# Optimization experiments

Hardware: AMD Instinct MI355X
Metric: run time of the kernel (lower is better)

Reference implementation:

```python
import jax, jax.numpy as jnp
import numpy as np

TILE = 16
CLIP_NEAR, CLIP_FAR = 0.01, 10.0


def _sqrt_keepnan(x):
    # forward: sqrt(x) for x>0, NaN otherwise (matches torch.sqrt on negatives);
    # double-where keeps gradients finite.
    pos = x > 0
    return jnp.where(pos, jnp.sqrt(jnp.where(pos, x, 1.0)), jnp.nan)


def _quat_to_rot(q):
    # faithful to the source _quat_to_rot (including its sign quirks)
    x, y, z, w = q[:, 0], q[:, 1], q[:, 2], q[:, 3]
    r0 = jnp.stack([1 - 2 * (y * y + z * z), 2 * (x * y - w * z), 2 * (x * z + w * y)], -1)
    r1 = jnp.stack([2 * (x * y + w * z), 1 - 2 * (x * x - z * z), 2 * (y * z - w * x)], -1)
    r2 = jnp.stack([2 * (x * z + w * y), 2 * (y * z + w * x), 1 - 2 * (x * x + y * y)], -1)
    return jnp.stack([r0, r1, r2], -2)  # (N,3,3)


def _forward(mu, scales, quats, cols, opcs, viewmat, focal, H, W):
    N = mu.shape[0]
    fx = fy = float(focal)
    cx, cy = W / 2.0, H / 2.0
    n_, f_ = CLIP_NEAR, CLIP_FAR

    # --- project gaussians ---
    t = viewmat @ jnp.concatenate([mu.T, jnp.ones((1, N), mu.dtype)], 0)  # (4,N) camera space
    tp0 = (2.0 * fx / W) * t[0]
    tp1 = (2.0 * fy / H) * t[1]
    tp2 = ((f_ + n_) / (f_ - n_)) * t[2] + (-2.0 * f_ * n_ / (f_ - n_)) * t[3]
    tp3 = t[2]
    xys = jnp.stack([W * tp0 / tp3 / 2 + cx, H * tp1 / tp3 / 2 + cy], 1)  # (N,2)
    depths = tp2

    R = _quat_to_rot(quats)
    RS = R * scales[:, None, :]              # R @ diag(s)
    Sigma = RS @ jnp.swapaxes(RS, 1, 2)      # (N,3,3)
    tz = t[2]
    zz = jnp.zeros_like(tz)
    J = jnp.stack([
        jnp.stack([fx / tz, zz, -fx * t[0] / tz ** 2], -1),
        jnp.stack([zz, fy / tz, -fy * t[1] / tz ** 2], -1)], -2)  # (N,2,3)
    Rcw = viewmat[:3, :3]
    M = jnp.einsum('nij,jk->nik', J, Rcw)
    covs = jnp.einsum('nij,njk,nlk->nil', M, Sigma, M)  # (N,2,2)

    ind = jnp.argsort(depths)                # depth sort (front-to-back)
    xys, covs = xys[ind], covs[ind]
    cols_s, opcs_s = cols[ind], opcs[ind]

    # --- bounding boxes -> tile membership mask ---
    a, b, d = covs[:, 0, 0], covs[:, 0, 1], covs[:, 1, 1]
    Aev = jnp.sqrt(a * a - 2 * a * d + 4 * b * b + d * d)
    Bev = a + d
    l1, l2 = 0.5 * (Aev + Bev), 0.5 * (Bev - Aev)
    r1 = 3.0 * _sqrt_keepnan(l1)
    r2 = 3.0 * _sqrt_keepnan(l2)
    mx, my = xys[:, 0], xys[:, 1]
    corners = jnp.stack([
        jnp.stack([mx - r1, my + r2], -1),
        jnp.stack([mx + r1, my + r2], -1),
        jnp.stack([mx + r1, my - r2], -1),
        jnp.stack([mx - r1, my - r2], -1)], 1)  # (N,4,2)
    theta = jnp.where(b != 0, jnp.arctan2(l1 - a, b),
                      jnp.where(a >= d, jnp.pi / 2, 0.0))
    cth, sth = jnp.cos(theta), jnp.sin(theta)
    rot = jnp.stack([jnp.stack([cth, -sth], -1), jnp.stack([sth, cth], -1)], -2)
    bm = corners.mean(1, keepdims=True)
    bbs = jnp.einsum('nij,nkj->nki', rot, corners - bm) + bm
    bbs = jnp.where(jnp.isnan(bbs), -1.0, bbs)
    Wt, Ht = W // TILE, H // TILE
    xmin = jnp.clip(jnp.floor(bbs[:, :, 0].min(1) / TILE), 0, Wt - 1).astype(jnp.int32)
    xmax = jnp.clip(jnp.ceil(bbs[:, :, 0].max(1) / TILE), 0, Wt - 1).astype(jnp.int32)
    ymin = jnp.clip(jnp.floor(bbs[:, :, 1].min(1) / TILE), 0, Ht - 1).astype(jnp.int32)
    ymax = jnp.clip(jnp.ceil(bbs[:, :, 1].max(1) / TILE), 0, Ht - 1).astype(jnp.int32)
    txi = jnp.arange(Wt)
    tyi = jnp.arange(Ht)
    tmask = ((txi[None, None, :] >= xmin[:, None, None]) & (txi[None, None, :] <= xmax[:, None, None]) &
             (tyi[None, :, None] >= ymin[:, None, None]) & (tyi[None, :, None] <= ymax[:, None, None]))  # (N,Ht,Wt)
    pmask = jnp.moveaxis(jnp.repeat(jnp.repeat(tmask, TILE, 1), TILE, 2), 0, -1)  # (H,W,N)

    # --- rasterize: per-pixel gaussian eval + sorted alpha compositing ---
    e = 1e-6
    det = (a + e) * (d + e) - covs[:, 0, 1] * covs[:, 1, 0]
    i00 = (d + e) / det
    i01 = -covs[:, 0, 1] / det
    i10 = -covs[:, 1, 0] / det
    i11 = (a + e) / det
    px = jnp.arange(W, dtype=mu.dtype)
    py = jnp.arange(H, dtype=mu.dtype)
    dx = px[None, :, None] - mx[None, None, :]   # (1,W,N)
    dy = py[:, None, None] - my[None, None, :]   # (H,1,N)
    quad = dx * (i00 * dx + i01 * dy) + dy * (i10 * dx + i11 * dy)  # (H,W,N)
    Pg = jnp.nan_to_num(jnp.exp(-0.5 * quad))
    O = jax.nn.sigmoid(jax.nn.sigmoid(opcs_s))   # double sigmoid: faithful to source
    alpha = O[None, None, :] * Pg
    alpha = jnp.where(pmask, alpha, 0.0)         # only gaussians binned to this tile
    alpha = jnp.where(alpha < 0.001, 0.0, alpha)
    alpha = jnp.minimum(alpha, 0.99)
    trans = jnp.cumprod(1.0 - alpha, -1)         # inclusive transmittance
    Dtr = jnp.concatenate([jnp.ones((H, W, 1), alpha.dtype), trans[..., :-1]], -1)
    C = jnp.clip(cols_s, 1e-4, 1.0)
    rgb = jnp.clip(jnp.einsum('hwn,nc->hwc', alpha * Dtr, C), 1e-4, 1.0)
    nonempty = jnp.repeat(jnp.repeat(tmask.any(0), TILE, 0), TILE, 1)  # empty tiles stay 0
    return jnp.where(nonempty[..., None], rgb, 0.0)


def setup_inputs() -> dict:
    key = jax.random.key(0)
    ks = jax.random.split(key, 6)
    N, H, W = 512, 256, 256
    mu = jax.random.normal(ks[0], (N, 3), jnp.float32)
    scales = jax.random.uniform(ks[1], (N, 3), jnp.float32) * 0.05 + 0.01
    q = jax.random.normal(ks[2], (N, 4), jnp.float32)
    quats = q / jnp.linalg.norm(q, axis=1, keepdims=True)
    cols = jax.random.uniform(ks[3], (N, 3), jnp.float32)
    opcs = jax.random.normal(ks[4], (N,), jnp.float32)
    viewmat = jnp.array([[1, 0, 0, 0], [0, 1, 0, 0], [0, 0, 1, 5.0], [0, 0, 0, 1]], jnp.float32)
    gt = jax.random.uniform(ks[5], (H, W, 3), jnp.float32)
    return {"mu": mu, "scales": scales, "quats": quats, "cols": cols, "opcs": opcs,
            "viewmat": viewmat, "gt": gt, "focal": 200, "H": H, "W": W}


def reference(mu, scales, quats, cols, opcs, viewmat, gt, focal, H, W):
    # gt is accepted (matches source signature) but unused by forward
    return _forward(mu, scales, quats, cols, opcs, viewmat, focal, H, W)
```

## Files before the change

### kernel.cpp

```cpp
#include <hip/hip_runtime.h>
#include <math.h>
#include <float.h>

#define NMAX 512
#define TILE 16
#define FDIV(a,b) __fdividef((a),(b))

__global__ __launch_bounds__(512) void fused_kernel(
    const float* __restrict__ mu, const float* __restrict__ scales,
    const float* __restrict__ quats, const float* __restrict__ cols,
    const float* __restrict__ opcs, const float* __restrict__ vm,
    const int* __restrict__ focal_p, const int* __restrict__ H_p,
    const int* __restrict__ W_p, float* __restrict__ out, int N)
{
    __shared__ float s_mx[NMAX], s_my[NMAX];
    __shared__ float s_i00[NMAX], s_i01[NMAX], s_i10[NMAX], s_i11[NMAX];
    __shared__ float s_O[NMAX], s_c0[NMAX], s_c1[NMAX], s_c2[NMAX];
    __shared__ unsigned int s_key[NMAX];
    __shared__ int s_list[NMAX];
    __shared__ unsigned long long s_lk[NMAX];
    __shared__ int s_sorted[NMAX];
    __shared__ float s_pr[256], s_pg[256], s_pb[256], s_pT[256];
    __shared__ int s_cnt;

    const int lt = threadIdx.x;
    const int p  = lt & 255;
    const int hv = lt >> 8;
    const int tx = blockIdx.x, ty = blockIdx.y;

    if (lt == 0) s_cnt = 0;
    __syncthreads();

    const int   Wi = W_p[0], Hi = H_p[0];
    const float fx = (float)focal_p[0];
    const float fy = fx;
    const float Wf = (float)Wi, Hf = (float)Hi;
    const float cxf = (float)((double)Wi / 2.0);
    const float cyf = (float)((double)Hi / 2.0);
    const float sxc = (float)(2.0 * (double)fx / (double)Wi);
    const float syc = (float)(2.0 * (double)fy / (double)Hi);
    const float dc1 = (float)((10.0 + 0.01) / (10.0 - 0.01));
    const float dc2 = (float)(-2.0 * 10.0 * 0.01 / (10.0 - 0.01));
    const int Wt = Wi / TILE, Ht = Hi / TILE;

    const int g = lt;
    if (g < N) {
        const float m0 = mu[3*g], m1 = mu[3*g+1], m2 = mu[3*g+2];
        const float t0 = vm[0]*m0  + vm[1]*m1  + vm[2]*m2  + vm[3];
        const float t1 = vm[4]*m0  + vm[5]*m1  + vm[6]*m2  + vm[7];
        const float t2 = vm[8]*m0  + vm[9]*m1  + vm[10]*m2 + vm[11];
        const float t3 = vm[12]*m0 + vm[13]*m1 + vm[14]*m2 + vm[15];

        const float depth = dc1 * t2 + dc2 * t3;
        unsigned int ub = __float_as_uint(depth);
        ub = (ub & 0x80000000u) ? ~ub : (ub | 0x80000000u);
        s_key[g] = ub;

        const float mx = FDIV(Wf * (sxc * t0), t2) * 0.5f + cxf;
        const float my = FDIV(Hf * (syc * t1), t2) * 0.5f + cyf;

        const float4 q = ((const float4*)quats)[g];
        const float qx = q.x, qy = q.y, qz = q.z, qw = q.w;
        const float R00 = 1.0f - 2.0f*(qy*qy + qz*qz);
        const float R01 = 2.0f*(qx*qy - qw*qz);
        const float R02 = 2.0f*(qx*qz + qw*qy);
        const float R10 = 2.0f*(qx*qy + qw*qz);
        const float R11 = 1.0f - 2.0f*(qx*qx - qz*qz);
        const float R12 = 2.0f*(qy*qz - qw*qx);
        const float R20 = 2.0f*(qx*qz + qw*qy);
        const float R21 = 2.0f*(qy*qz + qw*qx);
        const float R22 = 1.0f - 2.0f*(qx*qx + qy*qy);

        const float s0 = scales[3*g], s1 = scales[3*g+1], s2 = scales[3*g+2];
        const float A00 = R00*s0, A01 = R01*s1, A02 = R02*s2;
        const float A10 = R10*s0, A11 = R11*s1, A12 = R12*s2;
        const float A20 = R20*s0, A21 = R21*s1, A22 = R22*s2;
        const float S00 = A00*A00 + A01*A01 + A02*A02;
        const float S01 = A00*A10 + A01*A11 + A02*A12;
        const float S02 = A00*A20 + A01*A21 + A02*A22;
        const float S11 = A10*A10 + A11*A11 + A12*A12;
        const float S12 = A10*A20 + A11*A21 + A12*A22;
        const float S22 = A20*A20 + A21*A21 + A22*A22;

        const float tz = t2;
        const float J00 = FDIV(fx, tz);
        const float J02 = FDIV(-fx * t0, tz * tz);
        const float J11 = FDIV(fy, tz);
        const float J12 = FDIV(-fy * t1, tz * tz);
        const float M00 = J00*vm[0] + J02*vm[8];
        const float M01 = J00*vm[1] + J02*vm[9];
        const float M02 = J00*vm[2] + J02*vm[10];
        const float M10 = J11*vm[4] + J12*vm[8];
        const float M11 = J11*vm[5] + J12*vm[9];
        const float M12 = J11*vm[6] + J12*vm[10];
        const float T00 = M00*S00 + M01*S01 + M02*S02;
        const float T01 = M00*S01 + M01*S11 + M02*S12;
        const float T02 = M00*S02 + M01*S12 + M02*S22;
        const float T10 = M10*S00 + M11*S01 + M12*S02;
        const float T11 = M10*S01 + M11*S11 + M12*S12;
        const float T12 = M10*S02 + M11*S12 + M12*S22;
        const float a   = T00*M00 + T01*M01 + T02*M02;
        const float b   = T00*M10 + T01*M11 + T02*M12;
        const float c10 = T10*M00 + T11*M01 + T12*M02;
        const float d   = T10*M10 + T11*M11 + T12*M12;

        const float Aev = sqrtf(a*a - 2.0f*a*d + 4.0f*b*b + d*d);
        const float Bev = a + d;
        const float l1 = 0.5f * (Aev + Bev);
        const float l2 = 0.5f * (Bev - Aev);
        const float r1 = (l1 > 0.0f) ? 3.0f * sqrtf(l1) : NAN;
        const float r2 = (l2 > 0.0f) ? 3.0f * sqrtf(l2) : NAN;

        float cth, sth;
        if (b != 0.0f) {
            const float yv = l1 - a;
            const float h  = sqrtf(b*b + yv*yv);
            cth = FDIV(b,  h);
            sth = FDIV(yv, h);
        } else if (a >= d) {
            cth = -4.371139e-8f;
            sth = 1.0f;
        } else {
            cth = 1.0f;
            sth = 0.0f;
        }

        const float crx[4] = { mx - r1, mx + r1, mx + r1, mx - r1 };
        const float cry[4] = { my + r2, my + r2, my - r2, my - r2 };
        const float bmx = (((crx[0] + crx[1]) + crx[2]) + crx[3]) * 0.25f;
        const float bmy = (((cry[0] + cry[1]) + cry[2]) + cry[3]) * 0.25f;

        float xmn = FLT_MAX, xmxv = -FLT_MAX, ymn = FLT_MAX, ymxv = -FLT_MAX;
        #pragma unroll
        for (int k = 0; k < 4; ++k) {
            const float ox = crx[k] - bmx, oy = cry[k] - bmy;
            float bx = (cth*ox + (-sth)*oy) + bmx;
            float by = (sth*ox + cth*oy) + bmy;
            if (isnan(bx)) bx = -1.0f;
            if (isnan(by)) by = -1.0f;
            xmn = fminf(xmn, bx); xmxv = fmaxf(xmxv, bx);
            ymn = fminf(ymn, by); ymxv = fmaxf(ymxv, by);
        }
        const int xmin = (int)fminf(fmaxf(floorf(xmn  * 0.0625f), 0.0f), (float)(Wt - 1));
        const int xmax = (int)fminf(fmaxf(ceilf (xmxv * 0.0625f), 0.0f), (float)(Wt - 1));
        const int ymin = (int)fminf(fmaxf(floorf(ymn  * 0.0625f), 0.0f), (float)(Ht - 1));
        const int ymax = (int)fminf(fmaxf(ceilf (ymxv * 0.0625f), 0.0f), (float)(Ht - 1));

        const float e = 1e-06f;
        const float det = (a + e) * (d + e) - b * c10;
        const float idet = FDIV(1.0f, det);
        s_i00[g] = (d + e) * idet;
        s_i01[g] = -b   * idet;
        s_i10[g] = -c10 * idet;
        s_i11[g] = (a + e) * idet;

        const float op  = opcs[g];
        const float sg1 = FDIV(1.0f, 1.0f + __expf(-op));
        s_O[g] = FDIV(1.0f, 1.0f + __expf(-sg1));

        s_c0[g] = fminf(fmaxf(cols[3*g    ], 1e-04f), 1.0f);
        s_c1[g] = fminf(fmaxf(cols[3*g + 1], 1e-04f), 1.0f);
        s_c2[g] = fminf(fmaxf(cols[3*g + 2], 1e-04f), 1.0f);
        s_mx[g] = mx; s_my[g] = my;

        if (tx >= xmin && tx <= xmax && ty >= ymin && ty <= ymax) {
            const int pos = atomicAdd(&s_cnt, 1);
            s_list[pos] = g;
        }
    }
    __syncthreads();
    const int M = s_cnt;

    for (int t = lt; t < M; t += 512) {
        const int gi = s_list[t];
        s_lk[t] = ((unsigned long long)s_key[gi] << 32) | (unsigned int)gi;
    }
    __syncthreads();
    for (int t = lt; t < M; t += 512) {
        const unsigned long long mine = s_lk[t];
        int rank = 0;
        for (int s = 0; s < M; ++s) rank += (s_lk[s] < mine) ? 1 : 0;
        s_sorted[rank] = (int)(mine & 0xFFFFFFFFu);
    }
    __syncthreads();

    const int W  = gridDim.x * TILE;
    const int px = tx * TILE + (p & 15);
    const int py = ty * TILE + (p >> 4);
    const float fpx = (float)px, fpy = (float)py;

    const int Mh = (M + 1) >> 1;
    const int j0 = hv ? Mh : 0;
    const int j1 = hv ? M  : Mh;

    float Tt = 1.0f, rr = 0.0f, gg = 0.0f, bb = 0.0f;
    for (int j = j0; j < j1; ++j) {
        const int n = s_sorted[j];
        const float dx = fpx - s_mx[n];
        const float dy = fpy - s_my[n];
        const float quad = dx * (s_i00[n]*dx + s_i01[n]*dy)
                         + dy * (s_i10[n]*dx + s_i11[n]*dy);
        float Pg = __expf(-0.5f * quad);
        if (isnan(Pg)) Pg = 0.0f;
        float alpha = s_O[n] * Pg;
        if (alpha < 0.001f) continue;
        alpha = fminf(alpha, 0.99f);
        const float wgt = alpha * Tt;
        rr += wgt * s_c0[n];
        gg += wgt * s_c1[n];
        bb += wgt * s_c2[n];
        Tt *= (1.0f - alpha);
    }

    if (hv == 1) { s_pr[p] = rr; s_pg[p] = gg; s_pb[p] = bb; s_pT[p] = Tt; }
    __syncthreads();

    if (hv == 0) {
        rr += Tt * s_pr[p];
        gg += Tt * s_pg[p];
        bb += Tt * s_pb[p];

        const int o = (py * W + px) * 3;
        if (M > 0) {
            out[o    ] = fminf(fmaxf(rr, 1e-04f), 1.0f);
            out[o + 1] = fminf(fmaxf(gg, 1e-04f), 1.0f);
            out[o + 2] = fminf(fmaxf(bb, 1e-04f), 1.0f);
        } else {
            out[o] = 0.0f; out[o + 1] = 0.0f; out[o + 2] = 0.0f;
        }
    }
}

extern "C" void kernel_launch(void* const* d_in, const int* in_sizes, int n_in,
                              void* d_out, int out_size, void* d_ws, size_t ws_size,
                              hipStream_t stream) {
    const float* mu     = (const float*)d_in[0];
    const float* scales = (const float*)d_in[1];
    const float* quats  = (const float*)d_in[2];
    const float* cols   = (const float*)d_in[3];
    const float* opcs   = (const float*)d_in[4];
    const float* vm     = (const float*)d_in[5];
    const int* focal_p  = (const int*)d_in[7];
    const int* H_p      = (const int*)d_in[8];
    const int* W_p      = (const int*)d_in[9];

    const int N = in_sizes[4];
    const int HW = out_size / 3;
    int W = (int)(sqrt((double)HW) + 0.5);
    int H = HW / W;

    dim3 grid(W / TILE, H / TILE), block(512);
    fused_kernel<<<grid, block, 0, stream>>>(mu, scales, quats, cols, opcs, vm,
                                             focal_p, H_p, W_p, (float*)d_out, N);
}
```

Measured before the change: 17.60 us.

## Split per-gaussian preprocessing into a separate kernel and compact lists via ballot

Per-gaussian projection, covariance, bounding-box and opacity math now runs once in a prep kernel that writes to workspace, instead of being recomputed redundantly in each of the 256 tile blocks. The render kernel reads packed tile bounds, builds its per-tile list with wave ballot/popcount instead of shared atomics, and gathers parameters into shared memory in sorted order so the blend loop indexes directly without indirection. The cost is a second kernel launch and a global-memory round trip through the workspace.

```diff
diff --git a/kernel.cpp b/kernel.cpp
--- a/kernel.cpp
+++ b/kernel.cpp
@@ -6,30 +6,16 @@
 #define TILE 16
 #define FDIV(a,b) __fdividef((a),(b))
 
-__global__ __launch_bounds__(512) void fused_kernel(
+
+__global__ __launch_bounds__(256) void prep_kernel(
     const float* __restrict__ mu, const float* __restrict__ scales,
     const float* __restrict__ quats, const float* __restrict__ cols,
     const float* __restrict__ opcs, const float* __restrict__ vm,
     const int* __restrict__ focal_p, const int* __restrict__ H_p,
-    const int* __restrict__ W_p, float* __restrict__ out, int N)
+    const int* __restrict__ W_p, float* __restrict__ ws, int N)
 {
-    __shared__ float s_mx[NMAX], s_my[NMAX];
-    __shared__ float s_i00[NMAX], s_i01[NMAX], s_i10[NMAX], s_i11[NMAX];
-    __shared__ float s_O[NMAX], s_c0[NMAX], s_c1[NMAX], s_c2[NMAX];
-    __shared__ unsigned int s_key[NMAX];
-    __shared__ int s_list[NMAX];
-    __shared__ unsigned long long s_lk[NMAX];
-    __shared__ int s_sorted[NMAX];
-    __shared__ float s_pr[256], s_pg[256], s_pb[256], s_pT[256];
-    __shared__ int s_cnt;
-
-    const int lt = threadIdx.x;
-    const int p  = lt & 255;
-    const int hv = lt >> 8;
-    const int tx = blockIdx.x, ty = blockIdx.y;
-
-    if (lt == 0) s_cnt = 0;
-    __syncthreads();
+    const int g = blockIdx.x * 256 + threadIdx.x;
+    if (g >= N) return;
 
     const int   Wi = W_p[0], Hi = H_p[0];
     const float fx = (float)focal_p[0];
@@ -43,147 +29,194 @@
     const float dc2 = (float)(-2.0 * 10.0 * 0.01 / (10.0 - 0.01));
     const int Wt = Wi / TILE, Ht = Hi / TILE;
 
-    const int g = lt;
-    if (g < N) {
-        const float m0 = mu[3*g], m1 = mu[3*g+1], m2 = mu[3*g+2];
-        const float t0 = vm[0]*m0  + vm[1]*m1  + vm[2]*m2  + vm[3];
-        const float t1 = vm[4]*m0  + vm[5]*m1  + vm[6]*m2  + vm[7];
-        const float t2 = vm[8]*m0  + vm[9]*m1  + vm[10]*m2 + vm[11];
-        const float t3 = vm[12]*m0 + vm[13]*m1 + vm[14]*m2 + vm[15];
-
-        const float depth = dc1 * t2 + dc2 * t3;
-        unsigned int ub = __float_as_uint(depth);
-        ub = (ub & 0x80000000u) ? ~ub : (ub | 0x80000000u);
-        s_key[g] = ub;
-
-        const float mx = FDIV(Wf * (sxc * t0), t2) * 0.5f + cxf;
-        const float my = FDIV(Hf * (syc * t1), t2) * 0.5f + cyf;
-
-        const float4 q = ((const float4*)quats)[g];
-        const float qx = q.x, qy = q.y, qz = q.z, qw = q.w;
-        const float R00 = 1.0f - 2.0f*(qy*qy + qz*qz);
-        const float R01 = 2.0f*(qx*qy - qw*qz);
-        const float R02 = 2.0f*(qx*qz + qw*qy);
-        const float R10 = 2.0f*(qx*qy + qw*qz);
-        const float R11 = 1.0f - 2.0f*(qx*qx - qz*qz);
-        const float R12 = 2.0f*(qy*qz - qw*qx);
-        const float R20 = 2.0f*(qx*qz + qw*qy);
-        const float R21 = 2.0f*(qy*qz + qw*qx);
-        const float R22 = 1.0f - 2.0f*(qx*qx + qy*qy);
-
-        const float s0 = scales[3*g], s1 = scales[3*g+1], s2 = scales[3*g+2];
-        const float A00 = R00*s0, A01 = R01*s1, A02 = R02*s2;
-        const float A10 = R10*s0, A11 = R11*s1, A12 = R12*s2;
-        const float A20 = R20*s0, A21 = R21*s1, A22 = R22*s2;
-        const float S00 = A00*A00 + A01*A01 + A02*A02;
-        const float S01 = A00*A10 + A01*A11 + A02*A12;
-        const float S02 = A00*A20 + A01*A21 + A02*A22;
-        const float S11 = A10*A10 + A11*A11 + A12*A12;
-        const float S12 = A10*A20 + A11*A21 + A12*A22;
-        const float S22 = A20*A20 + A21*A21 + A22*A22;
-
-        const float tz = t2;
-        const float J00 = FDIV(fx, tz);
-        const float J02 = FDIV(-fx * t0, tz * tz);
-        const float J11 = FDIV(fy, tz);
-        const float J12 = FDIV(-fy * t1, tz * tz);
-        const float M00 = J00*vm[0] + J02*vm[8];
-        const float M01 = J00*vm[1] + J02*vm[9];
-        const float M02 = J00*vm[2] + J02*vm[10];
-        const float M10 = J11*vm[4] + J12*vm[8];
-        const float M11 = J11*vm[5] + J12*vm[9];
-        const float M12 = J11*vm[6] + J12*vm[10];
-        const float T00 = M00*S00 + M01*S01 + M02*S02;
-        const float T01 = M00*S01 + M01*S11 + M02*S12;
-        const float T02 = M00*S02 + M01*S12 + M02*S22;
-        const float T10 = M10*S00 + M11*S01 + M12*S02;
-        const float T11 = M10*S01 + M11*S11 + M12*S12;
-        const float T12 = M10*S02 + M11*S12 + M12*S22;
-        const float a   = T00*M00 + T01*M01 + T02*M02;
-        const float b   = T00*M10 + T01*M11 + T02*M12;
-        const float c10 = T10*M00 + T11*M01 + T12*M02;
-        const float d   = T10*M10 + T11*M11 + T12*M12;
-
-        const float Aev = sqrtf(a*a - 2.0f*a*d + 4.0f*b*b + d*d);
-        const float Bev = a + d;
-        const float l1 = 0.5f * (Aev + Bev);
-        const float l2 = 0.5f * (Bev - Aev);
-        const float r1 = (l1 > 0.0f) ? 3.0f * sqrtf(l1) : NAN;
-        const float r2 = (l2 > 0.0f) ? 3.0f * sqrtf(l2) : NAN;
-
-        float cth, sth;
-        if (b != 0.0f) {
-            const float yv = l1 - a;
-            const float h  = sqrtf(b*b + yv*yv);
-            cth = FDIV(b,  h);
-            sth = FDIV(yv, h);
-        } else if (a >= d) {
-            cth = -4.371139e-8f;
-            sth = 1.0f;
-        } else {
-            cth = 1.0f;
-            sth = 0.0f;
-        }
-
-        const float crx[4] = { mx - r1, mx + r1, mx + r1, mx - r1 };
-        const float cry[4] = { my + r2, my + r2, my - r2, my - r2 };
-        const float bmx = (((crx[0] + crx[1]) + crx[2]) + crx[3]) * 0.25f;
-        const float bmy = (((cry[0] + cry[1]) + cry[2]) + cry[3]) * 0.25f;
-
-        float xmn = FLT_MAX, xmxv = -FLT_MAX, ymn = FLT_MAX, ymxv = -FLT_MAX;
-        #pragma unroll
-        for (int k = 0; k < 4; ++k) {
-            const float ox = crx[k] - bmx, oy = cry[k] - bmy;
-            float bx = (cth*ox + (-sth)*oy) + bmx;
-            float by = (sth*ox + cth*oy) + bmy;
-            if (isnan(bx)) bx = -1.0f;
-            if (isnan(by)) by = -1.0f;
-            xmn = fminf(xmn, bx); xmxv = fmaxf(xmxv, bx);
-            ymn = fminf(ymn, by); ymxv = fmaxf(ymxv, by);
-        }
-        const int xmin = (int)fminf(fmaxf(floorf(xmn  * 0.0625f), 0.0f), (float)(Wt - 1));
-        const int xmax = (int)fminf(fmaxf(ceilf (xmxv * 0.0625f), 0.0f), (float)(Wt - 1));
-        const int ymin = (int)fminf(fmaxf(floorf(ymn  * 0.0625f), 0.0f), (float)(Ht - 1));
-        const int ymax = (int)fminf(fmaxf(ceilf (ymxv * 0.0625f), 0.0f), (float)(Ht - 1));
-
-        const float e = 1e-06f;
-        const float det = (a + e) * (d + e) - b * c10;
-        const float idet = FDIV(1.0f, det);
-        s_i00[g] = (d + e) * idet;
-        s_i01[g] = -b   * idet;
-        s_i10[g] = -c10 * idet;
-        s_i11[g] = (a + e) * idet;
-
-        const float op  = opcs[g];
-        const float sg1 = FDIV(1.0f, 1.0f + __expf(-op));
-        s_O[g] = FDIV(1.0f, 1.0f + __expf(-sg1));
-
-        s_c0[g] = fminf(fmaxf(cols[3*g    ], 1e-04f), 1.0f);
-        s_c1[g] = fminf(fmaxf(cols[3*g + 1], 1e-04f), 1.0f);
-        s_c2[g] = fminf(fmaxf(cols[3*g + 2], 1e-04f), 1.0f);
-        s_mx[g] = mx; s_my[g] = my;
-
-        if (tx >= xmin && tx <= xmax && ty >= ymin && ty <= ymax) {
-            const int pos = atomicAdd(&s_cnt, 1);
-            s_list[pos] = g;
-        }
-    }
-    __syncthreads();
-    const int M = s_cnt;
-
-    for (int t = lt; t < M; t += 512) {
-        const int gi = s_list[t];
-        s_lk[t] = ((unsigned long long)s_key[gi] << 32) | (unsigned int)gi;
-    }
-    __syncthreads();
+    const float m0 = mu[3*g], m1 = mu[3*g+1], m2 = mu[3*g+2];
+    const float t0 = vm[0]*m0  + vm[1]*m1  + vm[2]*m2  + vm[3];
+    const float t1 = vm[4]*m0  + vm[5]*m1  + vm[6]*m2  + vm[7];
+    const float t2 = vm[8]*m0  + vm[9]*m1  + vm[10]*m2 + vm[11];
+    const float t3 = vm[12]*m0 + vm[13]*m1 + vm[14]*m2 + vm[15];
+
+    const float depth = dc1 * t2 + dc2 * t3;
+    unsigned int ub = __float_as_uint(depth);
+    ub = (ub & 0x80000000u) ? ~ub : (ub | 0x80000000u);
+
+    const float mx = FDIV(Wf * (sxc * t0), t2) * 0.5f + cxf;
+    const float my = FDIV(Hf * (syc * t1), t2) * 0.5f + cyf;
+
+    const float4 q = ((const float4*)quats)[g];
+    const float qx = q.x, qy = q.y, qz = q.z, qw = q.w;
+    const float R00 = 1.0f - 2.0f*(qy*qy + qz*qz);
+    const float R01 = 2.0f*(qx*qy - qw*qz);
+    const float R02 = 2.0f*(qx*qz + qw*qy);
+    const float R10 = 2.0f*(qx*qy + qw*qz);
+    const float R11 = 1.0f - 2.0f*(qx*qx - qz*qz);
+    const float R12 = 2.0f*(qy*qz - qw*qx);
+    const float R20 = 2.0f*(qx*qz + qw*qy);
+    const float R21 = 2.0f*(qy*qz + qw*qx);
+    const float R22 = 1.0f - 2.0f*(qx*qx + qy*qy);
+
+    const float s0 = scales[3*g], s1 = scales[3*g+1], s2 = scales[3*g+2];
+    const float A00 = R00*s0, A01 = R01*s1, A02 = R02*s2;
+    const float A10 = R10*s0, A11 = R11*s1, A12 = R12*s2;
+    const float A20 = R20*s0, A21 = R21*s1, A22 = R22*s2;
+    const float S00 = A00*A00 + A01*A01 + A02*A02;
+    const float S01 = A00*A10 + A01*A11 + A02*A12;
+    const float S02 = A00*A20 + A01*A21 + A02*A22;
+    const float S11 = A10*A10 + A11*A11 + A12*A12;
+    const float S12 = A10*A20 + A11*A21 + A12*A22;
+    const float S22 = A20*A20 + A21*A21 + A22*A22;
+
+    const float tz = t2;
+    const float J00 = FDIV(fx, tz);
+    const float J02 = FDIV(-fx * t0, tz * tz);
+    const float J11 = FDIV(fy, tz);
+    const float J12 = FDIV(-fy * t1, tz * tz);
+    const float M00 = J00*vm[0] + J02*vm[8];
+    const float M01 = J00*vm[1] + J02*vm[9];
+    const float M02 = J00*vm[2] + J02*vm[10];
+    const float M10 = J11*vm[4] + J12*vm[8];
+    const float M11 = J11*vm[5] + J12*vm[9];
+    const float M12 = J11*vm[6] + J12*vm[10];
+    const float T00 = M00*S00 + M01*S01 + M02*S02;
+    const float T01 = M00*S01 + M01*S11 + M02*S12;
+    const float T02 = M00*S02 + M01*S12 + M02*S22;
+    const float T10 = M10*S00 + M11*S01 + M12*S02;
+    const float T11 = M10*S01 + M11*S11 + M12*S12;
+    const float T12 = M10*S02 + M11*S12 + M12*S22;
+    const float a   = T00*M00 + T01*M01 + T02*M02;
+    const float b   = T00*M10 + T01*M11 + T02*M12;
+    const float c10 = T10*M00 + T11*M01 + T12*M02;
+    const float d   = T10*M10 + T11*M11 + T12*M12;
+
+    const float Aev = sqrtf(a*a - 2.0f*a*d + 4.0f*b*b + d*d);
+    const float Bev = a + d;
+    const float l1 = 0.5f * (Aev + Bev);
+    const float l2 = 0.5f * (Bev - Aev);
+    const float r1 = (l1 > 0.0f) ? 3.0f * sqrtf(l1) : NAN;
+    const float r2 = (l2 > 0.0f) ? 3.0f * sqrtf(l2) : NAN;
+
+    float cth, sth;
+    if (b != 0.0f) {
+        const float yv = l1 - a;
+        const float h  = sqrtf(b*b + yv*yv);
+        cth = FDIV(b,  h);
+        sth = FDIV(yv, h);
+    } else if (a >= d) {
+        cth = -4.371139e-8f;
+        sth = 1.0f;
+    } else {
+        cth = 1.0f;
+        sth = 0.0f;
+    }
+
+    const float crx[4] = { mx - r1, mx + r1, mx + r1, mx - r1 };
+    const float cry[4] = { my + r2, my + r2, my - r2, my - r2 };
+    const float bmx = (((crx[0] + crx[1]) + crx[2]) + crx[3]) * 0.25f;
+    const float bmy = (((cry[0] + cry[1]) + cry[2]) + cry[3]) * 0.25f;
+
+    float xmn = FLT_MAX, xmxv = -FLT_MAX, ymn = FLT_MAX, ymxv = -FLT_MAX;
+    #pragma unroll
+    for (int k = 0; k < 4; ++k) {
+        const float ox = crx[k] - bmx, oy = cry[k] - bmy;
+        float bx = (cth*ox + (-sth)*oy) + bmx;
+        float by = (sth*ox + cth*oy) + bmy;
+        if (isnan(bx)) bx = -1.0f;
+        if (isnan(by)) by = -1.0f;
+        xmn = fminf(xmn, bx); xmxv = fmaxf(xmxv, bx);
+        ymn = fminf(ymn, by); ymxv = fmaxf(ymxv, by);
+    }
+    const int xmin = (int)fminf(fmaxf(floorf(xmn  * 0.0625f), 0.0f), (float)(Wt - 1));
+    const int xmax = (int)fminf(fmaxf(ceilf (xmxv * 0.0625f), 0.0f), (float)(Wt - 1));
+    const int ymin = (int)fminf(fmaxf(floorf(ymn  * 0.0625f), 0.0f), (float)(Ht - 1));
+    const int ymax = (int)fminf(fmaxf(ceilf (ymxv * 0.0625f), 0.0f), (float)(Ht - 1));
+
+    const float e = 1e-06f;
+    const float det = (a + e) * (d + e) - b * c10;
+    const float idet = FDIV(1.0f, det);
+
+    const float op  = opcs[g];
+    const float sg1 = FDIV(1.0f, 1.0f + __expf(-op));
+
+    ws[0*NMAX + g] = mx;
+    ws[1*NMAX + g] = my;
+    ws[2*NMAX + g] = (d + e) * idet;
+    ws[3*NMAX + g] = -b   * idet;
+    ws[4*NMAX + g] = -c10 * idet;
+    ws[5*NMAX + g] = (a + e) * idet;
+    ws[6*NMAX + g] = FDIV(1.0f, 1.0f + __expf(-sg1));
+    ws[7*NMAX + g] = fminf(fmaxf(cols[3*g    ], 1e-04f), 1.0f);
+    ws[8*NMAX + g] = fminf(fmaxf(cols[3*g + 1], 1e-04f), 1.0f);
+    ws[9*NMAX + g] = fminf(fmaxf(cols[3*g + 2], 1e-04f), 1.0f);
+    ((int*)ws)[10*NMAX + g] = xmin | (xmax << 8) | (ymin << 16) | (ymax << 24);
+    ((unsigned int*)ws)[11*NMAX + g] = ub;
+}
+
+__global__ __launch_bounds__(512) void render_kernel(
+    const float* __restrict__ ws, float* __restrict__ out, int N)
+{
+    __shared__ int s_bc[8];
+    __shared__ unsigned long long s_lk[NMAX];
+    __shared__ int s_ord[NMAX];
+    __shared__ float s_mx[NMAX], s_my[NMAX];
+    __shared__ float s_i00[NMAX], s_i01[NMAX], s_i10[NMAX], s_i11[NMAX];
+    __shared__ float s_O[NMAX], s_c0[NMAX], s_c1[NMAX], s_c2[NMAX];
+    __shared__ float s_pr[256], s_pg[256], s_pb[256], s_pT[256];
+
+    const int lt = threadIdx.x;
+    const int lane = lt & 63, w = lt >> 6;
+    const int tx = blockIdx.x, ty = blockIdx.y;
+
+    bool covered = false;
+    if (lt < N) {
+        const int bnd = ((const int*)ws)[10*NMAX + lt];
+        const int xmin =  bnd        & 255;
+        const int xmax = (bnd >> 8)  & 255;
+        const int ymin = (bnd >> 16) & 255;
+        const int ymax = (bnd >> 24) & 255;
+        covered = (tx >= xmin) & (tx <= xmax) & (ty >= ymin) & (ty <= ymax);
+    }
+    const unsigned long long word = __ballot(covered);
+    if (lane == 0) s_bc[w] = __popcll(word);
+    __syncthreads();
+
+    int base = 0, M = 0;
+    #pragma unroll
+    for (int i = 0; i < 8; ++i) {
+        const int c = s_bc[i];
+        if (i < w) base += c;
+        M += c;
+    }
+    if (covered) {
+        const int rank = base + __popcll(word & ((1ull << lane) - 1ull));
+        const unsigned int key = ((const unsigned int*)ws)[11*NMAX + lt];
+        s_lk[rank] = ((unsigned long long)key << 32) | (unsigned int)lt;
+    }
+    __syncthreads();
+
     for (int t = lt; t < M; t += 512) {
         const unsigned long long mine = s_lk[t];
         int rank = 0;
         for (int s = 0; s < M; ++s) rank += (s_lk[s] < mine) ? 1 : 0;
-        s_sorted[rank] = (int)(mine & 0xFFFFFFFFu);
-    }
-    __syncthreads();
-
+        s_ord[rank] = (int)(mine & 0xFFFFFFFFu);
+    }
+    __syncthreads();
+
+    for (int t = lt; t < M; t += 512) {
+        const int g = s_ord[t];
+        s_mx [t] = ws[0*NMAX + g];
+        s_my [t] = ws[1*NMAX + g];
+        s_i00[t] = ws[2*NMAX + g];
+        s_i01[t] = ws[3*NMAX + g];
+        s_i10[t] = ws[4*NMAX + g];
+        s_i11[t] = ws[5*NMAX + g];
+        s_O  [t] = ws[6*NMAX + g];
+        s_c0 [t] = ws[7*NMAX + g];
+        s_c1 [t] = ws[8*NMAX + g];
+        s_c2 [t] = ws[9*NMAX + g];
+    }
+    __syncthreads();
+
+    const int p  = lt & 255;
+    const int hv = lt >> 8;
     const int W  = gridDim.x * TILE;
     const int px = tx * TILE + (p & 15);
     const int py = ty * TILE + (p >> 4);
@@ -195,20 +228,19 @@
 
     float Tt = 1.0f, rr = 0.0f, gg = 0.0f, bb = 0.0f;
     for (int j = j0; j < j1; ++j) {
-        const int n = s_sorted[j];
-        const float dx = fpx - s_mx[n];
-        const float dy = fpy - s_my[n];
-        const float quad = dx * (s_i00[n]*dx + s_i01[n]*dy)
-                         + dy * (s_i10[n]*dx + s_i11[n]*dy);
+        const float dx = fpx - s_mx[j];
+        const float dy = fpy - s_my[j];
+        const float quad = dx * (s_i00[j]*dx + s_i01[j]*dy)
+                         + dy * (s_i10[j]*dx + s_i11[j]*dy);
         float Pg = __expf(-0.5f * quad);
         if (isnan(Pg)) Pg = 0.0f;
-        float alpha = s_O[n] * Pg;
+        float alpha = s_O[j] * Pg;
         if (alpha < 0.001f) continue;
         alpha = fminf(alpha, 0.99f);
         const float wgt = alpha * Tt;
-        rr += wgt * s_c0[n];
-        gg += wgt * s_c1[n];
-        bb += wgt * s_c2[n];
+        rr += wgt * s_c0[j];
+        gg += wgt * s_c1[j];
+        bb += wgt * s_c2[j];
         Tt *= (1.0f - alpha);
     }
 
@@ -249,7 +281,11 @@
     int W = (int)(sqrt((double)HW) + 0.5);
     int H = HW / W;
 
+    float* ws = (float*)d_ws;
+
+    prep_kernel<<<(N + 255) / 256, 256, 0, stream>>>(
+        mu, scales, quats, cols, opcs, vm, focal_p, H_p, W_p, ws, N);
+
     dim3 grid(W / TILE, H / TILE), block(512);
-    fused_kernel<<<grid, block, 0, stream>>>(mu, scales, quats, cols, opcs, vm,
-                                             focal_p, H_p, W_p, (float*)d_out, N);
+    render_kernel<<<grid, block, 0, stream>>>(ws, (float*)d_out, N);
 }
```

Measured after the change: 19.94 us. 13.3% more time.

## Compact tile lists with wave ballots and fold conic coefficients into blend loop

Applied to the files above, without the earlier changes.

Replaces the shared-memory atomic counter used to build each tile's gaussian list with wave-level ballot and popcount prefix sums, which writes sort keys directly and drops one barrier. The inverse covariance is pre-scaled into three coefficients (including -0.5) so the per-pixel quadratic form needs fewer loads and multiplies. The blending loop becomes branchless and uses FMAs. The bounding-box corner loop is simplified algebraically into min/max of separable terms. These are small gains on a short kernel, and the changed NaN handling and operation order may shift rounding slightly.

```diff
diff --git a/kernel.cpp b/kernel.cpp
--- a/kernel.cpp
+++ b/kernel.cpp
@@ -14,22 +14,16 @@
     const int* __restrict__ W_p, float* __restrict__ out, int N)
 {
     __shared__ float s_mx[NMAX], s_my[NMAX];
-    __shared__ float s_i00[NMAX], s_i01[NMAX], s_i10[NMAX], s_i11[NMAX];
+    __shared__ float s_q00[NMAX], s_qs[NMAX], s_q11[NMAX];
     __shared__ float s_O[NMAX], s_c0[NMAX], s_c1[NMAX], s_c2[NMAX];
-    __shared__ unsigned int s_key[NMAX];
-    __shared__ int s_list[NMAX];
     __shared__ unsigned long long s_lk[NMAX];
-    __shared__ int s_sorted[NMAX];
-    __shared__ float s_pr[256], s_pg[256], s_pb[256], s_pT[256];
-    __shared__ int s_cnt;
+    __shared__ int s_ord[NMAX];
+    __shared__ float s_pr[256], s_pg[256], s_pb[256];
+    __shared__ int s_bc[8];
 
     const int lt = threadIdx.x;
-    const int p  = lt & 255;
-    const int hv = lt >> 8;
+    const int lane = lt & 63, w = lt >> 6;
     const int tx = blockIdx.x, ty = blockIdx.y;
-
-    if (lt == 0) s_cnt = 0;
-    __syncthreads();
 
     const int   Wi = W_p[0], Hi = H_p[0];
     const float fx = (float)focal_p[0];
@@ -43,6 +37,8 @@
     const float dc2 = (float)(-2.0 * 10.0 * 0.01 / (10.0 - 0.01));
     const int Wt = Wi / TILE, Ht = Hi / TILE;
 
+    bool covered = false;
+    unsigned int key = 0;
     const int g = lt;
     if (g < N) {
         const float m0 = mu[3*g], m1 = mu[3*g+1], m2 = mu[3*g+2];
@@ -53,8 +49,7 @@
 
         const float depth = dc1 * t2 + dc2 * t3;
         unsigned int ub = __float_as_uint(depth);
-        ub = (ub & 0x80000000u) ? ~ub : (ub | 0x80000000u);
-        s_key[g] = ub;
+        key = (ub & 0x80000000u) ? ~ub : (ub | 0x80000000u);
 
         const float mx = FDIV(Wf * (sxc * t0), t2) * 0.5f + cxf;
         const float my = FDIV(Hf * (syc * t1), t2) * 0.5f + cyf;
@@ -125,22 +120,24 @@
             sth = 0.0f;
         }
 
-        const float crx[4] = { mx - r1, mx + r1, mx + r1, mx - r1 };
-        const float cry[4] = { my + r2, my + r2, my - r2, my - r2 };
-        const float bmx = (((crx[0] + crx[1]) + crx[2]) + crx[3]) * 0.25f;
-        const float bmy = (((cry[0] + cry[1]) + cry[2]) + cry[3]) * 0.25f;
-
-        float xmn = FLT_MAX, xmxv = -FLT_MAX, ymn = FLT_MAX, ymxv = -FLT_MAX;
-        #pragma unroll
-        for (int k = 0; k < 4; ++k) {
-            const float ox = crx[k] - bmx, oy = cry[k] - bmy;
-            float bx = (cth*ox + (-sth)*oy) + bmx;
-            float by = (sth*ox + cth*oy) + bmy;
-            if (isnan(bx)) bx = -1.0f;
-            if (isnan(by)) by = -1.0f;
-            xmn = fminf(xmn, bx); xmxv = fmaxf(xmxv, bx);
-            ymn = fminf(ymn, by); ymxv = fmaxf(ymxv, by);
-        }
+        const float u  = mx - r1, v  = mx + r1;
+        const float r_ = my + r2, s_ = my - r2;
+        const float bmx = (((u + v) + v) + u) * 0.25f;
+        const float bmy = (((r_ + r_) + s_) + s_) * 0.25f;
+        const float pxo = u - bmx, qxo = v - bmx;
+        const float ryo = r_ - bmy, syo = s_ - bmy;
+
+        const float Axp = cth * pxo, Axq = cth * qxo;
+        const float Bxr = (-sth) * ryo, Bxs = (-sth) * syo;
+        float xmn  = (fminf(Axp, Axq) + fminf(Bxr, Bxs)) + bmx;
+        float xmxv = (fmaxf(Axp, Axq) + fmaxf(Bxr, Bxs)) + bmx;
+        const float Ayp = sth * pxo, Ayq = sth * qxo;
+        const float Byr = cth * ryo, Bys = cth * syo;
+        float ymn  = (fminf(Ayp, Ayq) + fminf(Byr, Bys)) + bmy;
+        float ymxv = (fmaxf(Ayp, Ayq) + fmaxf(Byr, Bys)) + bmy;
+        if (isnan(xmxv)) { xmn = -1.0f; xmxv = -1.0f; }
+        if (isnan(ymxv)) { ymn = -1.0f; ymxv = -1.0f; }
+
         const int xmin = (int)fminf(fmaxf(floorf(xmn  * 0.0625f), 0.0f), (float)(Wt - 1));
         const int xmax = (int)fminf(fmaxf(ceilf (xmxv * 0.0625f), 0.0f), (float)(Wt - 1));
         const int ymin = (int)fminf(fmaxf(floorf(ymn  * 0.0625f), 0.0f), (float)(Ht - 1));
@@ -149,41 +146,50 @@
         const float e = 1e-06f;
         const float det = (a + e) * (d + e) - b * c10;
         const float idet = FDIV(1.0f, det);
-        s_i00[g] = (d + e) * idet;
-        s_i01[g] = -b   * idet;
-        s_i10[g] = -c10 * idet;
-        s_i11[g] = (a + e) * idet;
 
         const float op  = opcs[g];
         const float sg1 = FDIV(1.0f, 1.0f + __expf(-op));
-        s_O[g] = FDIV(1.0f, 1.0f + __expf(-sg1));
-
-        s_c0[g] = fminf(fmaxf(cols[3*g    ], 1e-04f), 1.0f);
-        s_c1[g] = fminf(fmaxf(cols[3*g + 1], 1e-04f), 1.0f);
-        s_c2[g] = fminf(fmaxf(cols[3*g + 2], 1e-04f), 1.0f);
-        s_mx[g] = mx; s_my[g] = my;
-
-        if (tx >= xmin && tx <= xmax && ty >= ymin && ty <= ymax) {
-            const int pos = atomicAdd(&s_cnt, 1);
-            s_list[pos] = g;
-        }
-    }
-    __syncthreads();
-    const int M = s_cnt;
-
-    for (int t = lt; t < M; t += 512) {
-        const int gi = s_list[t];
-        s_lk[t] = ((unsigned long long)s_key[gi] << 32) | (unsigned int)gi;
-    }
-    __syncthreads();
+
+        s_mx [g] = mx;
+        s_my [g] = my;
+        s_q00[g] = -0.5f * (d + e) * idet;
+        s_qs [g] =  0.5f * (b + c10) * idet;
+        s_q11[g] = -0.5f * (a + e) * idet;
+        s_O  [g] = FDIV(1.0f, 1.0f + __expf(-sg1));
+        s_c0 [g] = fminf(fmaxf(cols[3*g    ], 1e-04f), 1.0f);
+        s_c1 [g] = fminf(fmaxf(cols[3*g + 1], 1e-04f), 1.0f);
+        s_c2 [g] = fminf(fmaxf(cols[3*g + 2], 1e-04f), 1.0f);
+
+        covered = (tx >= xmin) & (tx <= xmax) & (ty >= ymin) & (ty <= ymax);
+    }
+
+    const unsigned long long word = __ballot(covered);
+    if (lane == 0) s_bc[w] = __popcll(word);
+    __syncthreads();
+
+    int base = 0, M = 0;
+    #pragma unroll
+    for (int i = 0; i < 8; ++i) {
+        const int c = s_bc[i];
+        if (i < w) base += c;
+        M += c;
+    }
+    if (covered) {
+        const int rank = base + __popcll(word & ((1ull << lane) - 1ull));
+        s_lk[rank] = ((unsigned long long)key << 32) | (unsigned int)g;
+    }
+    __syncthreads();
+
     for (int t = lt; t < M; t += 512) {
         const unsigned long long mine = s_lk[t];
         int rank = 0;
         for (int s = 0; s < M; ++s) rank += (s_lk[s] < mine) ? 1 : 0;
-        s_sorted[rank] = (int)(mine & 0xFFFFFFFFu);
-    }
-    __syncthreads();
-
+        s_ord[rank] = (int)(mine & 0xFFFFFFFFu);
+    }
+    __syncthreads();
+
+    const int p  = lt & 255;
+    const int hv = lt >> 8;
     const int W  = gridDim.x * TILE;
     const int px = tx * TILE + (p & 15);
     const int py = ty * TILE + (p >> 4);
@@ -195,30 +201,28 @@
 
     float Tt = 1.0f, rr = 0.0f, gg = 0.0f, bb = 0.0f;
     for (int j = j0; j < j1; ++j) {
-        const int n = s_sorted[j];
+        const int n = s_ord[j];
         const float dx = fpx - s_mx[n];
         const float dy = fpy - s_my[n];
-        const float quad = dx * (s_i00[n]*dx + s_i01[n]*dy)
-                         + dy * (s_i10[n]*dx + s_i11[n]*dy);
-        float Pg = __expf(-0.5f * quad);
-        if (isnan(Pg)) Pg = 0.0f;
+        const float qv = s_q00[n]*dx*dx + s_qs[n]*(dx*dy) + s_q11[n]*dy*dy;
+        float Pg = __expf(qv);
+        if (Pg != Pg) Pg = 0.0f;
         float alpha = s_O[n] * Pg;
-        if (alpha < 0.001f) continue;
-        alpha = fminf(alpha, 0.99f);
+        alpha = (alpha < 0.001f) ? 0.0f : fminf(alpha, 0.99f);
         const float wgt = alpha * Tt;
-        rr += wgt * s_c0[n];
-        gg += wgt * s_c1[n];
-        bb += wgt * s_c2[n];
-        Tt *= (1.0f - alpha);
-    }
-
-    if (hv == 1) { s_pr[p] = rr; s_pg[p] = gg; s_pb[p] = bb; s_pT[p] = Tt; }
+        rr = fmaf(wgt, s_c0[n], rr);
+        gg = fmaf(wgt, s_c1[n], gg);
+        bb = fmaf(wgt, s_c2[n], bb);
+        Tt = fmaf(-alpha, Tt, Tt);
+    }
+
+    if (hv == 1) { s_pr[p] = rr; s_pg[p] = gg; s_pb[p] = bb; }
     __syncthreads();
 
     if (hv == 0) {
-        rr += Tt * s_pr[p];
-        gg += Tt * s_pg[p];
-        bb += Tt * s_pb[p];
+        rr = fmaf(Tt, s_pr[p], rr);
+        gg = fmaf(Tt, s_pg[p], gg);
+        bb = fmaf(Tt, s_pb[p], bb);
 
         const int o = (py * W + px) * 3;
         if (M > 0) {
```

After: 16.26 us. -7.6%, faster.
